# Optimization experiments

Hardware: AMD Instinct MI355X
Metric: run time of the kernel (lower is better)

Reference implementation:

```python
import jax, jax.numpy as jnp
import numpy as np

B, L, D, H = 4, 4096, 1024, 16
HD = D // H  # head_dim = 64
SCALE = 1.0 / np.sqrt(HD)


def setup_inputs() -> dict:
    key = jax.random.key(0)
    ks = jax.random.split(key, 6)
    x = jax.random.normal(ks[0], (B, L, D), dtype=jnp.float32)
    Wqkv_w = jax.random.normal(ks[1], (3 * D, D), dtype=jnp.float32) * (1.0 / np.sqrt(D))
    Wqkv_b = jax.random.normal(ks[2], (3 * D,), dtype=jnp.float32) * 0.02
    out_w = jax.random.normal(ks[3], (D, D), dtype=jnp.float32) * (1.0 / np.sqrt(D))
    out_b = jax.random.normal(ks[4], (D,), dtype=jnp.float32) * 0.02
    gamma_raw = jax.random.uniform(ks[5], (H,), dtype=jnp.float32, minval=0.0, maxval=2.0)
    return {"x": x, "Wqkv_w": Wqkv_w, "Wqkv_b": Wqkv_b,
            "out_w": out_w, "out_b": out_b, "gamma_raw": gamma_raw}


def reference(x, Wqkv_w, Wqkv_b, out_w, out_b, gamma_raw):
    b, l, dm = x.shape
    # qkv projection: [B, L, 3*D] -> [3, B, H, L, hd]
    qkv = x @ Wqkv_w.T + Wqkv_b
    qkv = qkv.reshape(b, l, 3, H, HD).transpose(2, 0, 3, 1, 4)
    q, k, v = qkv[0], qkv[1], qkv[2]      # each [B, H, L, hd]
    k = k * SCALE
    g = jax.nn.sigmoid(gamma_raw)          # [H]
    gb = g[None, :, None, None]            # broadcast over [B, H, hd, hd]

    # move time axis to front for scan: [L, B, H, hd]
    qT = q.transpose(2, 0, 1, 3)
    kT = k.transpose(2, 0, 1, 3)
    vT = v.transpose(2, 0, 1, 3)

    def step(state, qkv_t):
        q_t, k_t, v_t = qkv_t
        # S = gamma * S + v k^T
        state = gb * state + jnp.einsum('bhi,bhj->bhij', v_t, k_t)
        # y = S q
        y_t = jnp.einsum('bhij,bhj->bhi', state, q_t)
        return state, y_t

    state0 = jnp.zeros((b, H, HD, HD), dtype=x.dtype)
    _, y = jax.lax.scan(step, state0, (qT, kT, vT))  # y: [L, B, H, hd]

    y = y.transpose(1, 0, 2, 3).reshape(b, l, dm)    # [B, L, D]
    return y @ out_w.T + out_b
```

## Files before the change

### kernel.cpp

```cpp
#include <hip/hip_runtime.h>
#include <cstdint>
#include <cstddef>

#define B_    4
#define L_    4096
#define D_    1024
#define H_    16
#define HD_   64
#define ND3_  3072
#define M1_   16384
#define NCH_  64
#define CSZ_  64
#define SCALE_ 0.125f

typedef __attribute__((ext_vector_type(8))) __bf16 bf16x8;
typedef __attribute__((ext_vector_type(4))) float f32x4;
typedef __attribute__((ext_vector_type(4))) unsigned int uint4v;

__device__ __forceinline__ float u2f(unsigned int u) { return __builtin_bit_cast(float, u); }
__device__ __forceinline__ unsigned int f2u(float f) { return __builtin_bit_cast(unsigned int, f); }
__device__ __forceinline__ float bf2f(unsigned short s) { return u2f(((unsigned int)s) << 16); }
__device__ __forceinline__ unsigned short f2bf(float f) {
  unsigned int u = f2u(f);
  u = u + 0x7fffu + ((u >> 16) & 1u);
  return (unsigned short)(u >> 16);
}

__device__ __forceinline__ void glds16(const unsigned short* g, unsigned short* l) {
  __builtin_amdgcn_global_load_lds(
      (const __attribute__((address_space(1))) void*)(uintptr_t)g,
      (__attribute__((address_space(3))) void*)(uintptr_t)l, 16, 0, 0);
}

__global__ __launch_bounds__(256) void cast3_kernel(
    const float* __restrict__ x, unsigned short* __restrict__ xo,
    const float* __restrict__ w1, unsigned short* __restrict__ w1o,
    const float* __restrict__ w2, unsigned short* __restrict__ w2o)
{
  const float* in; unsigned short* out; int i;
  int blk = blockIdx.x;
  if (blk < 16384)      { in = x;  out = xo;  i = (blk * 256 + threadIdx.x) * 4; }
  else if (blk < 19456) { in = w1; out = w1o; i = ((blk - 16384) * 256 + threadIdx.x) * 4; }
  else                  { in = w2; out = w2o; i = ((blk - 19456) * 256 + threadIdx.x) * 4; }
  float4 f = *(const float4*)(in + i);
  out[i + 0] = f2bf(f.x);
  out[i + 1] = f2bf(f.y);
  out[i + 2] = f2bf(f.z);
  out[i + 3] = f2bf(f.w);
}

template<int EPI>
__global__ __launch_bounds__(512, 2)
void gemm8(const unsigned short* __restrict__ A, const unsigned short* __restrict__ Bm,
           const float* __restrict__ bias,
           unsigned short* __restrict__ qo, unsigned short* __restrict__ ko,
           unsigned short* __restrict__ vo, float* __restrict__ Co,
           int M, int N, int K)
{
  __shared__ __align__(16) unsigned short Ab[2 * 2 * 8192];
  __shared__ __align__(16) unsigned short Bb[2 * 2 * 8192];

  const int nwg = gridDim.x;
  const int wg = (blockIdx.x & 7) * (nwg >> 3) + (blockIdx.x >> 3);
  const int nbn = N >> 8;
  const int bm = wg / nbn, bn = wg - bm * nbn;
  const int m0 = bm << 8, n0 = bn << 8;
  const int tid = threadIdx.x;
  const int lane = tid & 63, wid = tid >> 6;
  const int wr = wid >> 2, wc = wid & 3;
  const int fl = lane & 15, fh = lane >> 4;
  const int swz = fl & 7;

  const int nt = K >> 6;

  const int srow = lane >> 3;
  const int slc = (lane & 7) ^ srow;

  f32x4 acc[2][2][4][2] = {};

  auto stage = [&](const unsigned short* Mat, int rbase, int h, int kt,
                   unsigned short* buf) {
    const int d = kt & 1;
#pragma unroll
    for (int s = 0; s < 2; ++s) {
      const int rl = (wid * 2 + s) * 8 + srow;
      glds16(Mat + (size_t)(rbase + h * 128 + rl) * K + kt * 64 + slc * 8,
             buf + (d * 2 + h) * 8192 + (wid * 2 + s) * 512);
    }
  };

  stage(A, m0, 0, 0, Ab); stage(Bm, n0, 0, 0, Bb);
  stage(A, m0, 1, 0, Ab); stage(Bm, n0, 1, 0, Bb);
  stage(Bm, n0, 0, 1, Bb); stage(A, m0, 0, 1, Ab);
  asm volatile("s_waitcnt vmcnt(4)" ::: "memory");
  __builtin_amdgcn_s_barrier();
  __builtin_amdgcn_sched_barrier(0);

  for (int t = 0; t < nt; ++t) {
    const int d = t & 1;
    const unsigned short* Abuf = Ab + d * 16384;
    const unsigned short* Bbuf = Bb + d * 16384;
    bf16x8 af0[4][2], af1[4][2], bf0[2][2], bf1[2][2];

#pragma unroll
    for (int m = 0; m < 4; ++m)
#pragma unroll
      for (int ks = 0; ks < 2; ++ks)
        af0[m][ks] = *(const bf16x8*)(Abuf + (wr * 64 + m * 16 + fl) * 64 + ((ks * 4 + fh) ^ swz) * 8);
#pragma unroll
    for (int n = 0; n < 2; ++n)
#pragma unroll
      for (int ks = 0; ks < 2; ++ks)
        bf0[n][ks] = *(const bf16x8*)(Bbuf + (wc * 32 + n * 16 + fl) * 64 + ((ks * 4 + fh) ^ swz) * 8);
    if (t + 1 < nt) stage(A, m0, 1, t + 1, Ab);
    __builtin_amdgcn_s_barrier();
    asm volatile("s_waitcnt lgkmcnt(0)" ::: "memory");
    __builtin_amdgcn_sched_barrier(0);
    __builtin_amdgcn_s_setprio(1);
#pragma unroll
    for (int m = 0; m < 4; ++m)
#pragma unroll
      for (int n = 0; n < 2; ++n)
#pragma unroll
        for (int ks = 0; ks < 2; ++ks)
          acc[0][0][m][n] = __builtin_amdgcn_mfma_f32_16x16x32_bf16(af0[m][ks], bf0[n][ks], acc[0][0][m][n], 0, 0, 0);
    __builtin_amdgcn_s_setprio(0);
    __builtin_amdgcn_s_barrier();

#pragma unroll
    for (int m = 0; m < 4; ++m)
#pragma unroll
      for (int ks = 0; ks < 2; ++ks)
        af1[m][ks] = *(const bf16x8*)(Abuf + 8192 + (wr * 64 + m * 16 + fl) * 64 + ((ks * 4 + fh) ^ swz) * 8);
    if (t + 1 < nt) stage(Bm, n0, 1, t + 1, Bb);
    __builtin_amdgcn_s_barrier();
    asm volatile("s_waitcnt lgkmcnt(0)" ::: "memory");
    __builtin_amdgcn_sched_barrier(0);
    __builtin_amdgcn_s_setprio(1);
#pragma unroll
    for (int m = 0; m < 4; ++m)
#pragma unroll
      for (int n = 0; n < 2; ++n)
#pragma unroll
        for (int ks = 0; ks < 2; ++ks)
          acc[1][0][m][n] = __builtin_amdgcn_mfma_f32_16x16x32_bf16(af1[m][ks], bf0[n][ks], acc[1][0][m][n], 0, 0, 0);
    __builtin_amdgcn_s_setprio(0);
    __builtin_amdgcn_s_barrier();

#pragma unroll
    for (int n = 0; n < 2; ++n)
#pragma unroll
      for (int ks = 0; ks < 2; ++ks)
        bf1[n][ks] = *(const bf16x8*)(Bbuf + 8192 + (wc * 32 + n * 16 + fl) * 64 + ((ks * 4 + fh) ^ swz) * 8);
    if (t + 2 < nt) stage(Bm, n0, 0, t + 2, Bb);
    __builtin_amdgcn_s_barrier();
    asm volatile("s_waitcnt lgkmcnt(0)" ::: "memory");
    __builtin_amdgcn_sched_barrier(0);
    __builtin_amdgcn_s_setprio(1);
#pragma unroll
    for (int m = 0; m < 4; ++m)
#pragma unroll
      for (int n = 0; n < 2; ++n)
#pragma unroll
        for (int ks = 0; ks < 2; ++ks)
          acc[0][1][m][n] = __builtin_amdgcn_mfma_f32_16x16x32_bf16(af0[m][ks], bf1[n][ks], acc[0][1][m][n], 0, 0, 0);
    __builtin_amdgcn_s_setprio(0);
    __builtin_amdgcn_s_barrier();

    if (t + 2 < nt) stage(A, m0, 0, t + 2, Ab);
    __builtin_amdgcn_s_setprio(1);
#pragma unroll
    for (int m = 0; m < 4; ++m)
#pragma unroll
      for (int n = 0; n < 2; ++n)
#pragma unroll
        for (int ks = 0; ks < 2; ++ks)
          acc[1][1][m][n] = __builtin_amdgcn_mfma_f32_16x16x32_bf16(af1[m][ks], bf1[n][ks], acc[1][1][m][n], 0, 0, 0);
    __builtin_amdgcn_s_setprio(0);
    if (t < nt - 2) { asm volatile("s_waitcnt vmcnt(4)" ::: "memory"); }
    else            { asm volatile("s_waitcnt vmcnt(0)" ::: "memory"); }
    __builtin_amdgcn_s_barrier();
    __builtin_amdgcn_sched_barrier(0);
  }

  const int rb = fh << 2;
#pragma unroll
  for (int mh = 0; mh < 2; ++mh) {
#pragma unroll
    for (int nh = 0; nh < 2; ++nh) {
#pragma unroll
      for (int m = 0; m < 4; ++m) {
#pragma unroll
        for (int n = 0; n < 2; ++n) {
#pragma unroll
          for (int r = 0; r < 4; ++r) {
            int row = m0 + mh * 128 + wr * 64 + m * 16 + rb + r;
            int col = n0 + nh * 128 + wc * 32 + n * 16 + fl;
            float val = acc[mh][nh][m][n][r] + bias[col];
            if constexpr (EPI == 0) {
              int which = col >> 10;
              int hh = (col >> 6) & 15;
              int hd = col & 63;
              int bb = row >> 12;
              int tt2 = row & 4095;
              size_t idx = (((size_t)(bb * H_ + hh)) * L_ + tt2) * HD_ + hd;
              if (which == 0)      qo[idx] = f2bf(val);
              else if (which == 1) ko[idx] = f2bf(val * SCALE_);
              else                 vo[idx] = f2bf(val);
            } else {
              Co[(size_t)row * N + col] = val;
            }
          }
        }
      }
    }
  }
}

__global__ __launch_bounds__(256) void ret_phase1(
    const unsigned short* __restrict__ kb, const unsigned short* __restrict__ vb,
    const float* __restrict__ gamma_raw, unsigned short* __restrict__ Sbuf)
{
  int bhc = blockIdx.x;
  int c = bhc & 63, bh = bhc >> 6, h = bh & 15;
  float g = 1.f / (1.f + expf(-gamma_raw[h]));
  float lg2g = log2f(g);

  __shared__ __align__(16) unsigned short Kt[64][72];
  __shared__ __align__(16) unsigned short Vwt[64][72];

  int tid = threadIdx.x;
  size_t base = ((size_t)bh * L_ + (size_t)c * CSZ_) * HD_;
#pragma unroll
  for (int qq = 0; qq < 16; ++qq) {
    int e = tid + qq * 256;
    int j = e >> 6, col = e & 63;
    float wj = exp2f(lg2g * (float)(63 - j));
    Kt[col][j] = kb[base + e];
    Vwt[col][j] = f2bf(bf2f(vb[base + e]) * wj);
  }
  __syncthreads();

  int lane = tid & 63, w = tid >> 6;
  int fl = lane & 15, fh = lane >> 4;

  bf16x8 av0 = *(const bf16x8*)(&Vwt[w * 16 + fl][fh * 8]);
  bf16x8 av1 = *(const bf16x8*)(&Vwt[w * 16 + fl][32 + fh * 8]);

  int rb = fh << 2;
  unsigned short* out = Sbuf + (size_t)bhc * 4096;
#pragma unroll
  for (int jf = 0; jf < 4; ++jf) {
    bf16x8 bk0 = *(const bf16x8*)(&Kt[jf * 16 + fl][fh * 8]);
    bf16x8 bk1 = *(const bf16x8*)(&Kt[jf * 16 + fl][32 + fh * 8]);
    f32x4 z = {};
    z = __builtin_amdgcn_mfma_f32_16x16x32_bf16(av0, bk0, z, 0, 0, 0);
    z = __builtin_amdgcn_mfma_f32_16x16x32_bf16(av1, bk1, z, 0, 0, 0);
#pragma unroll
    for (int r = 0; r < 4; ++r) {
      int a = w * 16 + rb + r, bcol = jf * 16 + fl;
      out[a * 64 + bcol] = f2bf(z[r]);
    }
  }
}

__global__ __launch_bounds__(256) void ret_phase2(unsigned short* __restrict__ Sbuf,
                                                  const float* __restrict__ gamma_raw)
{
  int bh = blockIdx.x >> 3, grp = blockIdx.x & 7;
  int h = bh & 15;
  float g = 1.f / (1.f + expf(-gamma_raw[h]));
  float gC = powf(g, 64.f);
  int e = (grp * 256 + threadIdx.x) * 2;
  unsigned short* base = Sbuf + (size_t)bh * (NCH_ * 4096) + e;
  float s0 = 0.f, s1 = 0.f;
  for (int c = 0; c < NCH_; ++c) {
    unsigned int u = *(unsigned int*)(base + (size_t)c * 4096);
    float a0 = bf2f((unsigned short)(u & 0xffffu));
    float a1 = bf2f((unsigned short)(u >> 16));
    *(unsigned int*)(base + (size_t)c * 4096) =
        (unsigned int)f2bf(s0) | ((unsigned int)f2bf(s1) << 16);
    s0 = gC * s0 + a0;
    s1 = gC * s1 + a1;
  }
}

__global__ __launch_bounds__(256) void ret_phase3(
    const unsigned short* __restrict__ qb, const unsigned short* __restrict__ kb,
    const unsigned short* __restrict__ vb, const unsigned short* __restrict__ Sbuf,
    const float* __restrict__ gamma_raw, unsigned short* __restrict__ y)
{
  int bhc = blockIdx.x;
  int c = bhc & 63, bh = bhc >> 6, h = bh & 15, b = bh >> 4;
  float g = 1.f / (1.f + expf(-gamma_raw[h]));
  float lg2g = log2f(g);

  __shared__ __align__(16) unsigned short Qs[64][72];
  __shared__ __align__(16) unsigned short Ks[64][72];
  __shared__ __align__(16) unsigned short Vt[64][72];
  __shared__ __align__(16) unsigned short Sb[64][72];
  __shared__ __align__(16) unsigned short Ps[64][72];

  int tid = threadIdx.x;
  size_t base = ((size_t)bh * L_ + (size_t)c * CSZ_) * HD_;
  const unsigned short* Sp = Sbuf + (size_t)bhc * 4096;
#pragma unroll
  for (int qq = 0; qq < 16; ++qq) {
    int e = tid + qq * 256;
    int r = e >> 6, col = e & 63;
    Qs[r][col] = qb[base + e];
    Ks[r][col] = kb[base + e];
    Vt[col][r] = vb[base + e];
    Sb[r][col] = Sp[e];
  }
  __syncthreads();

  int lane = tid & 63, w = tid >> 6;
  int fl = lane & 15, fh = lane >> 4;
  int rb = fh << 2;

  bf16x8 aq0 = *(const bf16x8*)(&Qs[w * 16 + fl][fh * 8]);
  bf16x8 aq1 = *(const bf16x8*)(&Qs[w * 16 + fl][32 + fh * 8]);

  f32x4 pc[4], acc[4];
#pragma unroll
  for (int jf = 0; jf < 4; ++jf) {
    bf16x8 bk0 = *(const bf16x8*)(&Ks[jf * 16 + fl][fh * 8]);
    bf16x8 bk1 = *(const bf16x8*)(&Ks[jf * 16 + fl][32 + fh * 8]);
    f32x4 z = {};
    z = __builtin_amdgcn_mfma_f32_16x16x32_bf16(aq0, bk0, z, 0, 0, 0);
    z = __builtin_amdgcn_mfma_f32_16x16x32_bf16(aq1, bk1, z, 0, 0, 0);
    pc[jf] = z;

    bf16x8 bs0 = *(const bf16x8*)(&Sb[jf * 16 + fl][fh * 8]);
    bf16x8 bs1 = *(const bf16x8*)(&Sb[jf * 16 + fl][32 + fh * 8]);
    f32x4 zz = {};
    zz = __builtin_amdgcn_mfma_f32_16x16x32_bf16(aq0, bs0, zz, 0, 0, 0);
    zz = __builtin_amdgcn_mfma_f32_16x16x32_bf16(aq1, bs1, zz, 0, 0, 0);
    acc[jf] = zz;
  }

#pragma unroll
  for (int jf = 0; jf < 4; ++jf) {
#pragma unroll
    for (int r = 0; r < 4; ++r) {
      int i = w * 16 + rb + r, j = jf * 16 + fl;
      float val = (j <= i) ? pc[jf][r] * exp2f(lg2g * (float)(i - j)) : 0.f;
      Ps[i][j] = f2bf(val);
    }
  }

  float gi1[4];
#pragma unroll
  for (int r = 0; r < 4; ++r) gi1[r] = exp2f(lg2g * (float)(w * 16 + rb + r + 1));
#pragma unroll
  for (int jf = 0; jf < 4; ++jf)
#pragma unroll
    for (int r = 0; r < 4; ++r) acc[jf][r] *= gi1[r];

  __syncthreads();

  bf16x8 ap0 = *(const bf16x8*)(&Ps[w * 16 + fl][fh * 8]);
  bf16x8 ap1 = *(const bf16x8*)(&Ps[w * 16 + fl][32 + fh * 8]);
#pragma unroll
  for (int jf = 0; jf < 4; ++jf) {
    bf16x8 bv0 = *(const bf16x8*)(&Vt[jf * 16 + fl][fh * 8]);
    bf16x8 bv1 = *(const bf16x8*)(&Vt[jf * 16 + fl][32 + fh * 8]);
    acc[jf] = __builtin_amdgcn_mfma_f32_16x16x32_bf16(ap0, bv0, acc[jf], 0, 0, 0);
    acc[jf] = __builtin_amdgcn_mfma_f32_16x16x32_bf16(ap1, bv1, acc[jf], 0, 0, 0);
  }

  size_t yrow = ((size_t)(b * L_ + c * CSZ_)) * D_ + h * HD_;
#pragma unroll
  for (int jf = 0; jf < 4; ++jf) {
#pragma unroll
    for (int r = 0; r < 4; ++r) {
      int i = w * 16 + rb + r;
      y[yrow + (size_t)i * D_ + jf * 16 + fl] = f2bf(acc[jf][r]);
    }
  }
}

extern "C" void kernel_launch(void* const* d_in, const int* in_sizes, int n_in,
                              void* d_out, int out_size, void* d_ws, size_t ws_size,
                              hipStream_t stream)
{
  const float* x        = (const float*)d_in[0];
  const float* Wqkv_w   = (const float*)d_in[1];
  const float* Wqkv_b   = (const float*)d_in[2];
  const float* out_w    = (const float*)d_in[3];
  const float* out_b    = (const float*)d_in[4];
  const float* gamma_raw= (const float*)d_in[5];
  float* out = (float*)d_out;

  char* ws = (char*)d_ws;
  unsigned short* x_bf    = (unsigned short*)ws; ws += (size_t)16777216 * 2;
  unsigned short* wqkv_bf = (unsigned short*)ws; ws += (size_t)3145728 * 2;
  unsigned short* wout_bf = (unsigned short*)ws; ws += (size_t)1048576 * 2;
  unsigned short* qb      = (unsigned short*)ws; ws += (size_t)16777216 * 2;
  unsigned short* kb      = (unsigned short*)ws; ws += (size_t)16777216 * 2;
  unsigned short* vb      = (unsigned short*)ws; ws += (size_t)16777216 * 2;
  unsigned short* Sbuf    = (unsigned short*)ws; ws += (size_t)16777216 * 2;
  unsigned short* yb      = (unsigned short*)ws; ws += (size_t)16777216 * 2;

  cast3_kernel<<<20480, 256, 0, stream>>>(x, x_bf, Wqkv_w, wqkv_bf, out_w, wout_bf);

  gemm8<0><<<64 * 12, 512, 0, stream>>>(x_bf, wqkv_bf, Wqkv_b,
                                        qb, kb, vb, nullptr, M1_, ND3_, D_);

  ret_phase1<<<4096, 256, 0, stream>>>(kb, vb, gamma_raw, Sbuf);
  ret_phase2<<<512, 256, 0, stream>>>(Sbuf, gamma_raw);
  ret_phase3<<<4096, 256, 0, stream>>>(qb, kb, vb, Sbuf, gamma_raw, yb);

  gemm8<1><<<64 * 4, 512, 0, stream>>>(yb, wout_bf, out_b,
                                       nullptr, nullptr, nullptr, out, M1_, D_, D_);
}
```

Measured before the change: 233.3 us.

## Collapse four-phase GEMM main loop into one LDS-load then MFMA phase

Replaces the four interleaved sub-phases of the bf16 GEMM main loop with a single phase. Each iteration now issues both next-tile global-to-LDS stages, reads all A and B fragments from LDS, and waits once with a barrier. It then issues the t+2 stages and runs all 64 MFMAs back to back. The goal is fewer s_barrier and lgkmcnt waits per K-step. The cost is that LDS reads no longer overlap with MFMA work inside the iteration, and prefetch ordering changes.

```diff
diff --git a/kernel.cpp b/kernel.cpp
--- a/kernel.cpp
+++ b/kernel.cpp
@@ -91,7 +91,7 @@
 
   stage(A, m0, 0, 0, Ab); stage(Bm, n0, 0, 0, Bb);
   stage(A, m0, 1, 0, Ab); stage(Bm, n0, 1, 0, Bb);
-  stage(Bm, n0, 0, 1, Bb); stage(A, m0, 0, 1, Ab);
+  stage(A, m0, 0, 1, Ab); stage(Bm, n0, 0, 1, Bb);
   asm volatile("s_waitcnt vmcnt(4)" ::: "memory");
   __builtin_amdgcn_s_barrier();
   __builtin_amdgcn_sched_barrier(0);
@@ -102,81 +102,43 @@
     const unsigned short* Bbuf = Bb + d * 16384;
     bf16x8 af0[4][2], af1[4][2], bf0[2][2], bf1[2][2];
 
+    if (t + 1 < nt) { stage(A, m0, 1, t + 1, Ab); stage(Bm, n0, 1, t + 1, Bb); }
+
 #pragma unroll
     for (int m = 0; m < 4; ++m)
 #pragma unroll
-      for (int ks = 0; ks < 2; ++ks)
+      for (int ks = 0; ks < 2; ++ks) {
         af0[m][ks] = *(const bf16x8*)(Abuf + (wr * 64 + m * 16 + fl) * 64 + ((ks * 4 + fh) ^ swz) * 8);
+        af1[m][ks] = *(const bf16x8*)(Abuf + 8192 + (wr * 64 + m * 16 + fl) * 64 + ((ks * 4 + fh) ^ swz) * 8);
+      }
 #pragma unroll
     for (int n = 0; n < 2; ++n)
 #pragma unroll
-      for (int ks = 0; ks < 2; ++ks)
+      for (int ks = 0; ks < 2; ++ks) {
         bf0[n][ks] = *(const bf16x8*)(Bbuf + (wc * 32 + n * 16 + fl) * 64 + ((ks * 4 + fh) ^ swz) * 8);
-    if (t + 1 < nt) stage(A, m0, 1, t + 1, Ab);
+        bf1[n][ks] = *(const bf16x8*)(Bbuf + 8192 + (wc * 32 + n * 16 + fl) * 64 + ((ks * 4 + fh) ^ swz) * 8);
+      }
+
+    asm volatile("s_waitcnt lgkmcnt(0)" ::: "memory");
     __builtin_amdgcn_s_barrier();
-    asm volatile("s_waitcnt lgkmcnt(0)" ::: "memory");
     __builtin_amdgcn_sched_barrier(0);
+
+    if (t + 2 < nt) { stage(Bm, n0, 0, t + 2, Bb); stage(A, m0, 0, t + 2, Ab); }
+
     __builtin_amdgcn_s_setprio(1);
 #pragma unroll
     for (int m = 0; m < 4; ++m)
 #pragma unroll
       for (int n = 0; n < 2; ++n)
 #pragma unroll
-        for (int ks = 0; ks < 2; ++ks)
+        for (int ks = 0; ks < 2; ++ks) {
           acc[0][0][m][n] = __builtin_amdgcn_mfma_f32_16x16x32_bf16(af0[m][ks], bf0[n][ks], acc[0][0][m][n], 0, 0, 0);
+          acc[1][0][m][n] = __builtin_amdgcn_mfma_f32_16x16x32_bf16(af1[m][ks], bf0[n][ks], acc[1][0][m][n], 0, 0, 0);
+          acc[0][1][m][n] = __builtin_amdgcn_mfma_f32_16x16x32_bf16(af0[m][ks], bf1[n][ks], acc[0][1][m][n], 0, 0, 0);
+          acc[1][1][m][n] = __builtin_amdgcn_mfma_f32_16x16x32_bf16(af1[m][ks], bf1[n][ks], acc[1][1][m][n], 0, 0, 0);
+        }
     __builtin_amdgcn_s_setprio(0);
-    __builtin_amdgcn_s_barrier();
-
-#pragma unroll
-    for (int m = 0; m < 4; ++m)
-#pragma unroll
-      for (int ks = 0; ks < 2; ++ks)
-        af1[m][ks] = *(const bf16x8*)(Abuf + 8192 + (wr * 64 + m * 16 + fl) * 64 + ((ks * 4 + fh) ^ swz) * 8);
-    if (t + 1 < nt) stage(Bm, n0, 1, t + 1, Bb);
-    __builtin_amdgcn_s_barrier();
-    asm volatile("s_waitcnt lgkmcnt(0)" ::: "memory");
-    __builtin_amdgcn_sched_barrier(0);
-    __builtin_amdgcn_s_setprio(1);
-#pragma unroll
-    for (int m = 0; m < 4; ++m)
-#pragma unroll
-      for (int n = 0; n < 2; ++n)
-#pragma unroll
-        for (int ks = 0; ks < 2; ++ks)
-          acc[1][0][m][n] = __builtin_amdgcn_mfma_f32_16x16x32_bf16(af1[m][ks], bf0[n][ks], acc[1][0][m][n], 0, 0, 0);
-    __builtin_amdgcn_s_setprio(0);
-    __builtin_amdgcn_s_barrier();
-
-#pragma unroll
-    for (int n = 0; n < 2; ++n)
-#pragma unroll
-      for (int ks = 0; ks < 2; ++ks)
-        bf1[n][ks] = *(const bf16x8*)(Bbuf + 8192 + (wc * 32 + n * 16 + fl) * 64 + ((ks * 4 + fh) ^ swz) * 8);
-    if (t + 2 < nt) stage(Bm, n0, 0, t + 2, Bb);
-    __builtin_amdgcn_s_barrier();
-    asm volatile("s_waitcnt lgkmcnt(0)" ::: "memory");
-    __builtin_amdgcn_sched_barrier(0);
-    __builtin_amdgcn_s_setprio(1);
-#pragma unroll
-    for (int m = 0; m < 4; ++m)
-#pragma unroll
-      for (int n = 0; n < 2; ++n)
-#pragma unroll
-        for (int ks = 0; ks < 2; ++ks)
-          acc[0][1][m][n] = __builtin_amdgcn_mfma_f32_16x16x32_bf16(af0[m][ks], bf1[n][ks], acc[0][1][m][n], 0, 0, 0);
-    __builtin_amdgcn_s_setprio(0);
-    __builtin_amdgcn_s_barrier();
-
-    if (t + 2 < nt) stage(A, m0, 0, t + 2, Ab);
-    __builtin_amdgcn_s_setprio(1);
-#pragma unroll
-    for (int m = 0; m < 4; ++m)
-#pragma unroll
-      for (int n = 0; n < 2; ++n)
-#pragma unroll
-        for (int ks = 0; ks < 2; ++ks)
-          acc[1][1][m][n] = __builtin_amdgcn_mfma_f32_16x16x32_bf16(af1[m][ks], bf1[n][ks], acc[1][1][m][n], 0, 0, 0);
-    __builtin_amdgcn_s_setprio(0);
+
     if (t < nt - 2) { asm volatile("s_waitcnt vmcnt(4)" ::: "memory"); }
     else            { asm volatile("s_waitcnt vmcnt(0)" ::: "memory"); }
     __builtin_amdgcn_s_barrier();
```

After: 242.0 us. 3.7% more time.

## Rewrite QKV GEMM with 32x32x16 MFMA and triple-buffered K=32 staging

Applied to the files above, without the earlier changes.

Replaces the templated QKV projection GEMM with a dedicated kernel that uses 32x32x16 bf16 MFMA tiles (each wave computes 128x64) instead of 16x16x32. LDS staging changes to K-step 32 with a three-deep ring buffer and an XOR swizzle, and the A/B global-to-LDS loads are interleaved between the two MFMA sub-steps. The output GEMM is split into its own non-templated kernel with unchanged logic. The larger MFMA shape is meant to cut LDS read traffic per FLOP and raise MFMA efficiency. The trade-off is higher accumulator register pressure and a scattered bf16 store epilogue whose pattern now follows the 32x32 layout.

```diff
diff --git a/kernel.cpp b/kernel.cpp
--- a/kernel.cpp
+++ b/kernel.cpp
@@ -15,6 +15,7 @@
 
 typedef __attribute__((ext_vector_type(8))) __bf16 bf16x8;
 typedef __attribute__((ext_vector_type(4))) float f32x4;
+typedef __attribute__((ext_vector_type(16))) float f32x16;
 typedef __attribute__((ext_vector_type(4))) unsigned int uint4v;
 
 __device__ __forceinline__ float u2f(unsigned int u) { return __builtin_bit_cast(float, u); }
@@ -49,13 +50,123 @@
   out[i + 3] = f2bf(f.w);
 }
 
-template<int EPI>
 __global__ __launch_bounds__(512, 2)
-void gemm8(const unsigned short* __restrict__ A, const unsigned short* __restrict__ Bm,
-           const float* __restrict__ bias,
-           unsigned short* __restrict__ qo, unsigned short* __restrict__ ko,
-           unsigned short* __restrict__ vo, float* __restrict__ Co,
-           int M, int N, int K)
+void gemm_qkv(const unsigned short* __restrict__ A, const unsigned short* __restrict__ Bm,
+              const float* __restrict__ bias,
+              unsigned short* __restrict__ qo, unsigned short* __restrict__ ko,
+              unsigned short* __restrict__ vo, int M, int N, int K)
+{
+  constexpr int ASZ = 256 * 32, BSZ = 256 * 32;
+  __shared__ __align__(16) unsigned short Ab[3 * ASZ];
+  __shared__ __align__(16) unsigned short Bb[3 * BSZ];
+
+  const int nwg = gridDim.x;
+  const int wg = (blockIdx.x & 7) * (nwg >> 3) + (blockIdx.x >> 3);
+  const int nbn = N >> 8;
+  const int bm = wg / nbn, bn = wg - bm * nbn;
+  const int m0 = bm << 8, n0 = bn << 8;
+  const int tid = threadIdx.x;
+  const int lane = tid & 63, wid = tid >> 6;
+  const int wr = wid >> 2, wc = wid & 3;
+  const int fl = lane & 15;
+  const int l31 = lane & 31, l5 = lane >> 5;
+
+  const int rowbase = wid * 16 + (lane >> 2);
+  const int ckst = (lane & 3) ^ ((rowbase & 3) ^ ((rowbase >> 2) & 3));
+  const int sw = (fl & 3) ^ ((fl >> 2) & 3);
+
+  const int nt = K >> 5;
+
+  f32x16 acc[4][2] = {};
+
+  auto stageA = [&](int kt, int d) {
+#pragma unroll
+    for (int s = 0; s < 2; ++s)
+      glds16(A + (size_t)(m0 + s * 128 + rowbase) * K + kt * 32 + ckst * 8,
+             Ab + d * ASZ + s * 128 * 32 + wid * 512);
+  };
+  auto stageB = [&](int kt, int d) {
+#pragma unroll
+    for (int s = 0; s < 2; ++s)
+      glds16(Bm + (size_t)(n0 + s * 128 + rowbase) * K + kt * 32 + ckst * 8,
+             Bb + d * BSZ + s * 128 * 32 + wid * 512);
+  };
+
+  stageA(0, 0); stageB(0, 0);
+  stageA(1, 1); stageB(1, 1);
+
+  for (int t = 0; t < nt; ++t) {
+    const int d = t % 3;
+    if (t < nt - 1) { asm volatile("s_waitcnt vmcnt(4)" ::: "memory"); }
+    else            { asm volatile("s_waitcnt vmcnt(0)" ::: "memory"); }
+    __builtin_amdgcn_s_barrier();
+    __builtin_amdgcn_sched_barrier(0);
+
+    const unsigned short* Abuf = Ab + d * ASZ;
+    const unsigned short* Bbuf = Bb + d * BSZ;
+
+    {
+      const int ck = (0 * 2 + l5) ^ sw;
+      bf16x8 bfr[2], afr[4];
+#pragma unroll
+      for (int n = 0; n < 2; ++n)
+        bfr[n] = *(const bf16x8*)(Bbuf + (wc * 64 + n * 32 + l31) * 32 + ck * 8);
+#pragma unroll
+      for (int m = 0; m < 4; ++m)
+        afr[m] = *(const bf16x8*)(Abuf + (wr * 128 + m * 32 + l31) * 32 + ck * 8);
+      if (t + 2 < nt) stageA(t + 2, (t + 2) % 3);
+#pragma unroll
+      for (int m = 0; m < 4; ++m)
+#pragma unroll
+        for (int n = 0; n < 2; ++n)
+          acc[m][n] = __builtin_amdgcn_mfma_f32_32x32x16_bf16(afr[m], bfr[n], acc[m][n], 0, 0, 0);
+    }
+    {
+      const int ck = (1 * 2 + l5) ^ sw;
+      bf16x8 bfr[2], afr[4];
+#pragma unroll
+      for (int n = 0; n < 2; ++n)
+        bfr[n] = *(const bf16x8*)(Bbuf + (wc * 64 + n * 32 + l31) * 32 + ck * 8);
+#pragma unroll
+      for (int m = 0; m < 4; ++m)
+        afr[m] = *(const bf16x8*)(Abuf + (wr * 128 + m * 32 + l31) * 32 + ck * 8);
+      if (t + 2 < nt) stageB(t + 2, (t + 2) % 3);
+#pragma unroll
+      for (int m = 0; m < 4; ++m)
+#pragma unroll
+        for (int n = 0; n < 2; ++n)
+          acc[m][n] = __builtin_amdgcn_mfma_f32_32x32x16_bf16(afr[m], bfr[n], acc[m][n], 0, 0, 0);
+    }
+    __builtin_amdgcn_sched_barrier(0);
+  }
+
+#pragma unroll
+  for (int m = 0; m < 4; ++m) {
+#pragma unroll
+    for (int n = 0; n < 2; ++n) {
+#pragma unroll
+      for (int reg = 0; reg < 16; ++reg) {
+        int row = m0 + wr * 128 + m * 32 + (reg & 3) + 8 * (reg >> 2) + 4 * l5;
+        int col = n0 + wc * 64 + n * 32 + l31;
+        float val = acc[m][n][reg] + bias[col];
+        int which = col >> 10;
+        int hh = (col >> 6) & 15;
+        int hd = col & 63;
+        int bb = row >> 12;
+        int tt2 = row & 4095;
+        size_t idx = (((size_t)(bb * H_ + hh)) * L_ + tt2) * HD_ + hd;
+        if (which == 0)      qo[idx] = f2bf(val);
+        else if (which == 1) ko[idx] = f2bf(val * SCALE_);
+        else                 vo[idx] = f2bf(val);
+      }
+    }
+  }
+}
+
+__global__ __launch_bounds__(512, 2)
+void gemm_out8(const unsigned short* __restrict__ A, const unsigned short* __restrict__ Bm,
+               const float* __restrict__ bias, float* __restrict__ Co,
+               int M, int N, int K)
 {
   __shared__ __align__(16) unsigned short Ab[2 * 2 * 8192];
   __shared__ __align__(16) unsigned short Bb[2 * 2 * 8192];
@@ -185,36 +296,19 @@
 
   const int rb = fh << 2;
 #pragma unroll
-  for (int mh = 0; mh < 2; ++mh) {
-#pragma unroll
-    for (int nh = 0; nh < 2; ++nh) {
-#pragma unroll
-      for (int m = 0; m < 4; ++m) {
-#pragma unroll
-        for (int n = 0; n < 2; ++n) {
+  for (int mh = 0; mh < 2; ++mh)
+#pragma unroll
+    for (int nh = 0; nh < 2; ++nh)
+#pragma unroll
+      for (int m = 0; m < 4; ++m)
+#pragma unroll
+        for (int n = 0; n < 2; ++n)
 #pragma unroll
           for (int r = 0; r < 4; ++r) {
             int row = m0 + mh * 128 + wr * 64 + m * 16 + rb + r;
             int col = n0 + nh * 128 + wc * 32 + n * 16 + fl;
-            float val = acc[mh][nh][m][n][r] + bias[col];
-            if constexpr (EPI == 0) {
-              int which = col >> 10;
-              int hh = (col >> 6) & 15;
-              int hd = col & 63;
-              int bb = row >> 12;
-              int tt2 = row & 4095;
-              size_t idx = (((size_t)(bb * H_ + hh)) * L_ + tt2) * HD_ + hd;
-              if (which == 0)      qo[idx] = f2bf(val);
-              else if (which == 1) ko[idx] = f2bf(val * SCALE_);
-              else                 vo[idx] = f2bf(val);
-            } else {
-              Co[(size_t)row * N + col] = val;
-            }
+            Co[(size_t)row * N + col] = acc[mh][nh][m][n][r] + bias[col];
           }
-        }
-      }
-    }
-  }
 }
 
 __global__ __launch_bounds__(256) void ret_phase1(
@@ -405,13 +499,12 @@
 
   cast3_kernel<<<20480, 256, 0, stream>>>(x, x_bf, Wqkv_w, wqkv_bf, out_w, wout_bf);
 
-  gemm8<0><<<64 * 12, 512, 0, stream>>>(x_bf, wqkv_bf, Wqkv_b,
-                                        qb, kb, vb, nullptr, M1_, ND3_, D_);
+  gemm_qkv<<<64 * 12, 512, 0, stream>>>(x_bf, wqkv_bf, Wqkv_b,
+                                        qb, kb, vb, M1_, ND3_, D_);
 
   ret_phase1<<<4096, 256, 0, stream>>>(kb, vb, gamma_raw, Sbuf);
   ret_phase2<<<512, 256, 0, stream>>>(Sbuf, gamma_raw);
   ret_phase3<<<4096, 256, 0, stream>>>(qb, kb, vb, Sbuf, gamma_raw, yb);
 
-  gemm8<1><<<64 * 4, 512, 0, stream>>>(yb, wout_bf, out_b,
-                                       nullptr, nullptr, nullptr, out, M1_, D_, D_);
-}
+  gemm_out8<<<64 * 4, 512, 0, stream>>>(yb, wout_bf, out_b, out, M1_, D_, D_);
+}
```

After: 235.9 us. No clear change (+1.1%).
